# Performance work log

Measured on AMD Instinct MI355X. Metric: run time of the kernel, lower is better.

## Reference

```python
import jax, jax.numpy as jnp
import numpy as np
import math

B, T, M, C = 4, 2048, 16, 256   # batch, seq, m chunks, c_s chunk width
DIM = 1024                       # layer width; k = DIM // C = 4
D = 64                           # conditioning bottleneck
N_ITERS, TAU = 20, 1.0


def _diag_bias(rows, cols):
    b = np.full((rows, cols), -8.0, dtype=np.float32)
    for i in range(min(rows, cols)):
        b[i, i] = 0.0
    return jnp.asarray(b)


def setup_inputs() -> dict:
    key = jax.random.key(0)
    ks = jax.random.split(key, 10)
    state_dim = M * C
    k = DIM // C
    H_post = np.full((M, k), -8.0, dtype=np.float32)
    for i in range(M):
        H_post[i, i % k] = 0.0
    return {
        "s": jax.random.normal(ks[0], (B, T, M, C), jnp.float32),
        "gamma": 0.02 * jax.random.normal(ks[1], (state_dim,), jnp.float32),
        "compress": 0.02 * jax.random.normal(ks[2], (state_dim, D), jnp.float32),
        "alpha_pre": jnp.float32(0.01),
        "to_logits_pre": 0.02 * jax.random.normal(ks[3], (D, k * M), jnp.float32),
        "H_pre": _diag_bias(k, M),
        "alpha_align": jnp.float32(0.01),
        "to_logits_align": 0.02 * jax.random.normal(ks[4], (D, M * M), jnp.float32),
        "H_align": _diag_bias(M, M),
        "alpha_next": jnp.float32(0.01),
        "to_logits_next": 0.02 * jax.random.normal(ks[5], (D, M * M), jnp.float32),
        "H_next": _diag_bias(M, M),
        "alpha_post": jnp.float32(0.01),
        "to_logits_post": 0.02 * jax.random.normal(ks[6], (D, M * k), jnp.float32),
        "H_post": jnp.asarray(H_post),
        "W_layer": jax.random.normal(ks[7], (DIM, DIM), jnp.float32) / math.sqrt(DIM),
    }


def sinkhorn_log(logits, num_iters=N_ITERS, tau=TAU):
    """Log-domain Sinkhorn; output row-scaled so row sums = 1 * rows-normalized."""
    rows, cols = logits.shape[-2], logits.shape[-1]
    Z = logits / tau
    lr = -math.log(rows)
    lc = -math.log(cols)
    u0 = jnp.zeros(Z.shape[:-1], Z.dtype)
    v0 = jnp.zeros(Z.shape[:-2] + (cols,), Z.dtype)

    def body(_, uv):
        u, v = uv
        u = lr - jax.nn.logsumexp(Z + v[..., None, :], axis=-1)
        v = lc - jax.nn.logsumexp(Z + u[..., None], axis=-2)
        return (u, v)

    u, v = jax.lax.fori_loop(0, num_iters, body, (u0, v0))
    return jnp.exp(Z + u[..., None] + v[..., None, :]) * rows


def _route(code, alpha, to_logits, bias, state, rows, cols):
    """Fused: Sinkhorn(alpha*(code@to_logits)+bias) @ state."""
    raw = (code @ to_logits).reshape(code.shape[:-1] + (rows, cols))
    P = sinkhorn_log(alpha * raw + bias)
    return jnp.einsum('...ij,...jc->...ic', P, state)


def reference(s, gamma, compress, alpha_pre, to_logits_pre, H_pre,
              alpha_align, to_logits_align, H_align,
              alpha_next, to_logits_next, H_next,
              alpha_post, to_logits_post, H_post, W_layer):
    b, t, m, c = s.shape
    state_dim = m * c
    k = W_layer.shape[0] // c
    # RMSNorm over flattened state: F.normalize * sqrt(dim) * (gamma + 1)
    s_vec = s.reshape(b, t, state_dim)
    l2 = jnp.sqrt(jnp.sum(s_vec * s_vec, axis=-1, keepdims=True))
    s_norm = s_vec / jnp.maximum(l2, 1e-12) * jnp.sqrt(jnp.float32(state_dim)) * (gamma + 1.0)
    code = s_norm @ compress  # (b, t, d)
    # read: H_pre (k x m) routes state -> layer input
    layer_in = _route(code, alpha_pre, to_logits_pre, H_pre, s, k, m).reshape(b, t, k * c)
    layer_out = layer_in @ W_layer  # the wrapped layer_fn (dense linear)
    # write: align, absorb output via H_post, prepare next via H_next
    s_aligned = _route(code, alpha_align, to_logits_align, H_align, s, m, m)
    out_flat = layer_out.reshape(b, t, k, c)
    s_updated = s_aligned + _route(code, alpha_post, to_logits_post, H_post, out_flat, m, k)
    s_next = _route(code, alpha_next, to_logits_next, H_next, s_updated, m, m)
    return s_next
```

## Files before the change

### kernel.cpp

```cpp
#include <hip/hip_runtime.h>
#include <math.h>

#define NTOK 8192
#define SD   4096
#define ITERS 20

typedef __attribute__((ext_vector_type(8))) short short8;
typedef __attribute__((ext_vector_type(8))) unsigned short ushort8;
typedef __attribute__((ext_vector_type(4))) float f32x4;

__device__ inline unsigned short f2bf(float x) {
    unsigned int u = __float_as_uint(x);
    unsigned int r = (u + 0x7FFFu + ((u >> 16) & 1u)) >> 16;
    return (unsigned short)r;
}

__global__ __launch_bounds__(256) void k_prep(const float* __restrict__ compress,
                                              const float* __restrict__ gamma,
                                              unsigned short* __restrict__ cgT)
{
    __shared__ float tb[64][65];
    __shared__ float gsh[64];
    const int tid = threadIdx.x;
    const int k0 = blockIdx.x * 64;
    #pragma unroll 4
    for (int q = 0; q < 16; ++q) {
        const int idx = q * 256 + tid;
        const int r = idx >> 6, dd = idx & 63;
        tb[r][dd] = compress[(size_t)(k0 + r) * 64 + dd];
    }
    if (tid < 64) gsh[tid] = gamma[k0 + tid] + 1.0f;
    __syncthreads();
    #pragma unroll 4
    for (int q = 0; q < 16; ++q) {
        const int idx = q * 256 + tid;
        const int d = idx >> 6, r = idx & 63;
        cgT[(size_t)d * SD + k0 + r] = f2bf(tb[r][d] * gsh[r]);
    }
}

__global__ __launch_bounds__(256) void k_prept(const float* __restrict__ tl_pre,
                                               const float* __restrict__ tl_al,
                                               const float* __restrict__ tl_nx,
                                               const float* __restrict__ tl_po,
                                               unsigned short* __restrict__ tlT)
{
    const int idx = blockIdx.x * 256 + threadIdx.x;
    if (idx >= 640 * 64) return;
    const int k = idx / 640, n = idx - k * 640;
    float v;
    if (n < 64)       v = tl_pre[k * 64 + n];
    else if (n < 320) v = tl_al[k * 256 + (n - 64)];
    else if (n < 576) v = tl_nx[k * 256 + (n - 320)];
    else              v = tl_po[k * 64 + (n - 576)];
    tlT[(size_t)n * 64 + k] = f2bf(v);
}

__global__ __launch_bounds__(256) void k_code3(const float* __restrict__ s,
                                               const unsigned short* __restrict__ cgT,
                                               unsigned short* __restrict__ codeBF)
{
    __shared__ __align__(16) unsigned short s_sh[32 * 152];
    __shared__ __align__(16) unsigned short cg_sh[64 * 152];
    __shared__ float red[4 * 32 * 68];
    __shared__ float ssq_sh[32];
    const int tid  = threadIdx.x;
    const int lane = tid & 63;
    const int wid  = tid >> 6;
    const int tok0 = blockIdx.x * 32;
    const int st_tok = tid >> 3, st_k = (tid & 7) * 16;
    const int sg_d   = tid >> 2, sg_k = (tid & 3) * 32;
    const int wk = wid * 32;

    float ssq = 0.f;
    f32x4 acc[2][4];
    #pragma unroll
    for (int mi = 0; mi < 2; ++mi)
        #pragma unroll
        for (int ni = 0; ni < 4; ++ni) acc[mi][ni] = (f32x4){0.f, 0.f, 0.f, 0.f};

    for (int ks = 0; ks < 32; ++ks) {
        const int kg = ks * 128;
        __syncthreads();
        {
            const float4* sp = (const float4*)(s + (size_t)(tok0 + st_tok) * SD + kg + st_k);
            float4 v0 = sp[0], v1 = sp[1], v2 = sp[2], v3 = sp[3];
            ssq += v0.x*v0.x + v0.y*v0.y + v0.z*v0.z + v0.w*v0.w
                 + v1.x*v1.x + v1.y*v1.y + v1.z*v1.z + v1.w*v1.w
                 + v2.x*v2.x + v2.y*v2.y + v2.z*v2.z + v2.w*v2.w
                 + v3.x*v3.x + v3.y*v3.y + v3.z*v3.z + v3.w*v3.w;
            ushort8 lo, hi;
            lo[0]=f2bf(v0.x); lo[1]=f2bf(v0.y); lo[2]=f2bf(v0.z); lo[3]=f2bf(v0.w);
            lo[4]=f2bf(v1.x); lo[5]=f2bf(v1.y); lo[6]=f2bf(v1.z); lo[7]=f2bf(v1.w);
            hi[0]=f2bf(v2.x); hi[1]=f2bf(v2.y); hi[2]=f2bf(v2.z); hi[3]=f2bf(v2.w);
            hi[4]=f2bf(v3.x); hi[5]=f2bf(v3.y); hi[6]=f2bf(v3.z); hi[7]=f2bf(v3.w);
            ushort8* sw = (ushort8*)(s_sh + st_tok * 152 + st_k);
            sw[0] = lo; sw[1] = hi;
        }
        {
            const ushort8* gp = (const ushort8*)(cgT + (size_t)sg_d * SD + kg + sg_k);
            ushort8 c0 = gp[0], c1 = gp[1], c2 = gp[2], c3 = gp[3];
            ushort8* cw = (ushort8*)(cg_sh + sg_d * 152 + sg_k);
            cw[0] = c0; cw[1] = c1; cw[2] = c2; cw[3] = c3;
        }
        __syncthreads();

        short8 a[2], b[4];
        #pragma unroll
        for (int mi = 0; mi < 2; ++mi)
            a[mi] = *(const short8*)(s_sh + (mi * 16 + (lane & 15)) * 152 + wk + (lane >> 4) * 8);
        #pragma unroll
        for (int ni = 0; ni < 4; ++ni)
            b[ni] = *(const short8*)(cg_sh + (ni * 16 + (lane & 15)) * 152 + wk + (lane >> 4) * 8);
        #pragma unroll
        for (int mi = 0; mi < 2; ++mi)
            #pragma unroll
            for (int ni = 0; ni < 4; ++ni)
                acc[mi][ni] = __builtin_amdgcn_mfma_f32_16x16x32_bf16(a[mi], b[ni], acc[mi][ni], 0, 0, 0);
    }

    ssq += __shfl_xor(ssq, 1);
    ssq += __shfl_xor(ssq, 2);
    ssq += __shfl_xor(ssq, 4);
    if ((tid & 7) == 0) ssq_sh[st_tok] = ssq;

    #pragma unroll
    for (int mi = 0; mi < 2; ++mi)
        #pragma unroll
        for (int ni = 0; ni < 4; ++ni)
            #pragma unroll
            for (int r = 0; r < 4; ++r)
                red[wid * 2176 + (mi * 16 + (lane >> 4) * 4 + r) * 68 + ni * 16 + (lane & 15)] = acc[mi][ni][r];
    __syncthreads();
    if (tid < 32) ssq_sh[tid] = 64.0f / fmaxf(sqrtf(ssq_sh[tid]), 1e-12f);
    __syncthreads();

    #pragma unroll
    for (int q = 0; q < 8; ++q) {
        const int idx = q * 256 + tid;
        const int tok = idx >> 6, d = idx & 63;
        float v = red[0 * 2176 + tok * 68 + d] + red[1 * 2176 + tok * 68 + d]
                + red[2 * 2176 + tok * 68 + d] + red[3 * 2176 + tok * 68 + d];
        codeBF[(size_t)(tok0 + tok) * 64 + d] = f2bf(v * ssq_sh[tok]);
    }
}

__global__ __launch_bounds__(256) void k_logits(const unsigned short* __restrict__ codeBF,
                                                const unsigned short* __restrict__ tlT,
                                                float* __restrict__ logits)
{
    const int tid  = threadIdx.x;
    const int lane = tid & 63;
    const int wid  = tid >> 6;
    const int m0 = blockIdx.y * 64 + wid * 16;
    const int n0 = blockIdx.x * 128;

    f32x4 acc[8];
    #pragma unroll
    for (int ni = 0; ni < 8; ++ni) acc[ni] = (f32x4){0.f, 0.f, 0.f, 0.f};

    #pragma unroll
    for (int ks = 0; ks < 2; ++ks) {
        const int ko = ks * 32 + (lane >> 4) * 8;
        short8 a = *(const short8*)(codeBF + (size_t)(m0 + (lane & 15)) * 64 + ko);
        short8 b[8];
        #pragma unroll
        for (int ni = 0; ni < 8; ++ni)
            b[ni] = *(const short8*)(tlT + (size_t)(n0 + ni * 16 + (lane & 15)) * 64 + ko);
        #pragma unroll
        for (int ni = 0; ni < 8; ++ni)
            acc[ni] = __builtin_amdgcn_mfma_f32_16x16x32_bf16(a, b[ni], acc[ni], 0, 0, 0);
    }
    #pragma unroll
    for (int ni = 0; ni < 8; ++ni)
        #pragma unroll
        for (int r = 0; r < 4; ++r)
            logits[(size_t)(m0 + (lane >> 4) * 4 + r) * 640 + n0 + ni * 16 + (lane & 15)] = acc[ni][r];
}

__global__ __launch_bounds__(256) void k_sink(const float* __restrict__ logits,
                                              const float* __restrict__ a_pre_p, const float* __restrict__ H_pre,
                                              const float* __restrict__ a_al_p,  const float* __restrict__ H_al,
                                              const float* __restrict__ a_nx_p,  const float* __restrict__ H_nx,
                                              const float* __restrict__ a_po_p,  const float* __restrict__ H_po,
                                              float* __restrict__ Ppre,
                                              float* __restrict__ Pna, float* __restrict__ Pnp)
{
    __shared__ float Pal_sh[16 * 260];
    __shared__ float Pnx_sh[16 * 260];
    __shared__ float Ppo_sh[16 * 68];
    const int tid  = threadIdx.x;
    const int lane = tid & 63;
    const int wid  = tid >> 6;
    const int tok0 = blockIdx.x * 16;
    const int t_in = lane >> 2;
    const int sub  = lane & 3;
    const int tok  = tok0 + t_in;

    if (wid < 2) {
        const float alpha = (wid == 0) ? (*a_al_p) : (*a_nx_p);
        const float* Hp   = ((wid == 0) ? H_al : H_nx) + sub * 64;
        const float* lgp  = logits + (size_t)tok * 640 + (wid == 0 ? 64 : 320) + sub * 64;
        float Km[4][16];
        #pragma unroll
        for (int rr = 0; rr < 4; ++rr)
            #pragma unroll
            for (int c4 = 0; c4 < 4; ++c4) {
                float4 rv = *(const float4*)(lgp + rr * 16 + c4 * 4);
                float4 hv = *(const float4*)(Hp  + rr * 16 + c4 * 4);
                Km[rr][c4*4+0] = expf(alpha * rv.x + hv.x);
                Km[rr][c4*4+1] = expf(alpha * rv.y + hv.y);
                Km[rr][c4*4+2] = expf(alpha * rv.z + hv.z);
                Km[rr][c4*4+3] = expf(alpha * rv.w + hv.w);
            }
        float v[16], u[4];
        #pragma unroll
        for (int c = 0; c < 16; ++c) v[c] = 1.0f;
        for (int it = 0; it < ITERS; ++it) {
            #pragma unroll
            for (int rr = 0; rr < 4; ++rr) {
                float su = 0.f;
                #pragma unroll
                for (int c = 0; c < 16; ++c) su += Km[rr][c] * v[c];
                u[rr] = 0.0625f * __builtin_amdgcn_rcpf(su);
            }
            float pv[16];
            #pragma unroll
            for (int c = 0; c < 16; ++c)
                pv[c] = Km[0][c]*u[0] + Km[1][c]*u[1] + Km[2][c]*u[2] + Km[3][c]*u[3];
            #pragma unroll
            for (int c = 0; c < 16; ++c) pv[c] += __shfl_xor(pv[c], 1);
            #pragma unroll
            for (int c = 0; c < 16; ++c) pv[c] += __shfl_xor(pv[c], 2);
            #pragma unroll
            for (int c = 0; c < 16; ++c) v[c] = 0.0625f * __builtin_amdgcn_rcpf(pv[c]);
        }
        float* dst = ((wid == 0) ? Pal_sh : Pnx_sh) + t_in * 260;
        #pragma unroll
        for (int rr = 0; rr < 4; ++rr) {
            const float su16 = 16.0f * u[rr];
            #pragma unroll
            for (int c = 0; c < 16; ++c)
                dst[(sub * 4 + rr) * 16 + c] = Km[rr][c] * su16 * v[c];
        }
    } else if (wid == 2) {
        const float alpha = *a_pre_p;
        const float* lgp = logits + (size_t)tok * 640 + sub * 16;
        const float* Hp  = H_pre + sub * 16;
        float Km[16];
        #pragma unroll
        for (int c4 = 0; c4 < 4; ++c4) {
            float4 rv = *(const float4*)(lgp + c4 * 4);
            float4 hv = *(const float4*)(Hp  + c4 * 4);
            Km[c4*4+0] = expf(alpha * rv.x + hv.x);
            Km[c4*4+1] = expf(alpha * rv.y + hv.y);
            Km[c4*4+2] = expf(alpha * rv.z + hv.z);
            Km[c4*4+3] = expf(alpha * rv.w + hv.w);
        }
        float v[16], u;
        #pragma unroll
        for (int c = 0; c < 16; ++c) v[c] = 1.0f;
        for (int it = 0; it < ITERS; ++it) {
            float su = 0.f;
            #pragma unroll
            for (int c = 0; c < 16; ++c) su += Km[c] * v[c];
            u = 0.25f * __builtin_amdgcn_rcpf(su);
            float pv[16];
            #pragma unroll
            for (int c = 0; c < 16; ++c) pv[c] = Km[c] * u;
            #pragma unroll
            for (int c = 0; c < 16; ++c) pv[c] += __shfl_xor(pv[c], 1);
            #pragma unroll
            for (int c = 0; c < 16; ++c) pv[c] += __shfl_xor(pv[c], 2);
            #pragma unroll
            for (int c = 0; c < 16; ++c) v[c] = 0.0625f * __builtin_amdgcn_rcpf(pv[c]);
        }
        const float su4 = 4.0f * u;
        #pragma unroll
        for (int c = 0; c < 16; ++c)
            Ppre[(size_t)tok * 64 + sub * 16 + c] = Km[c] * su4 * v[c];
    } else {
        const float alpha = *a_po_p;
        const float* lgp = logits + (size_t)tok * 640 + 576 + sub * 16;
        const float* Hp  = H_po + sub * 16;
        float Km[4][4];
        #pragma unroll
        for (int rr = 0; rr < 4; ++rr) {
            float4 rv = *(const float4*)(lgp + rr * 4);
            float4 hv = *(const float4*)(Hp  + rr * 4);
            Km[rr][0] = expf(alpha * rv.x + hv.x);
            Km[rr][1] = expf(alpha * rv.y + hv.y);
            Km[rr][2] = expf(alpha * rv.z + hv.z);
            Km[rr][3] = expf(alpha * rv.w + hv.w);
        }
        float v[4], u[4];
        #pragma unroll
        for (int c = 0; c < 4; ++c) v[c] = 1.0f;
        for (int it = 0; it < ITERS; ++it) {
            #pragma unroll
            for (int rr = 0; rr < 4; ++rr) {
                float su = 0.f;
                #pragma unroll
                for (int c = 0; c < 4; ++c) su += Km[rr][c] * v[c];
                u[rr] = 0.0625f * __builtin_amdgcn_rcpf(su);
            }
            float pv[4];
            #pragma unroll
            for (int c = 0; c < 4; ++c)
                pv[c] = Km[0][c]*u[0] + Km[1][c]*u[1] + Km[2][c]*u[2] + Km[3][c]*u[3];
            #pragma unroll
            for (int c = 0; c < 4; ++c) pv[c] += __shfl_xor(pv[c], 1);
            #pragma unroll
            for (int c = 0; c < 4; ++c) pv[c] += __shfl_xor(pv[c], 2);
            #pragma unroll
            for (int c = 0; c < 4; ++c) v[c] = 0.25f * __builtin_amdgcn_rcpf(pv[c]);
        }
        #pragma unroll
        for (int rr = 0; rr < 4; ++rr) {
            const float su16 = 16.0f * u[rr];
            #pragma unroll
            for (int c = 0; c < 4; ++c)
                Ppo_sh[t_in * 68 + (sub * 4 + rr) * 4 + c] = Km[rr][c] * su16 * v[c];
        }
    }
    __syncthreads();

    const int ct = tid >> 4;
    const int cj = tid & 15;
    const float* pnx = Pnx_sh + ct * 260;
    const float* pal = Pal_sh + ct * 260;
    const float* ppo = Ppo_sh + ct * 68;
    #pragma unroll
    for (int m = 0; m < 16; ++m) {
        float acc = 0.f;
        #pragma unroll
        for (int t2 = 0; t2 < 16; ++t2) acc += pnx[m * 16 + t2] * pal[t2 * 16 + cj];
        Pna[(size_t)(tok0 + ct) * 256 + m * 16 + cj] = acc;
    }
    #pragma unroll
    for (int e = 0; e < 4; ++e) {
        const int idx = cj * 4 + e;
        const int m = idx >> 2, q = idx & 3;
        float acc = 0.f;
        #pragma unroll
        for (int t2 = 0; t2 < 16; ++t2) acc += pnx[m * 16 + t2] * ppo[t2 * 4 + q];
        Pnp[(size_t)(tok0 + ct) * 64 + idx] = acc;
    }
}

__global__ __launch_bounds__(256) void k_apply(const float* __restrict__ s,
                                               const float* __restrict__ Ppre,
                                               unsigned short* __restrict__ layer_in)
{
    __shared__ float Ppre_sh[64];
    const int tid = threadIdx.x;
    const int tok = blockIdx.x;
    float sreg[16];
    #pragma unroll
    for (int j = 0; j < 16; ++j) sreg[j] = s[(size_t)tok * SD + j * 256 + tid];
    if (tid < 64) Ppre_sh[tid] = Ppre[(size_t)tok * 64 + tid];
    __syncthreads();
    #pragma unroll
    for (int i = 0; i < 4; ++i) {
        float acc = 0.f;
        #pragma unroll
        for (int j = 0; j < 16; ++j) acc += Ppre_sh[i * 16 + j] * sreg[j];
        layer_in[(size_t)tok * 1024 + i * 256 + tid] = f2bf(acc);
    }
}

__global__ __launch_bounds__(256) void k_wt(const float* __restrict__ W,
                                            unsigned short* __restrict__ WT)
{
    __shared__ float tb[64][65];
    const int k0 = blockIdx.y * 64, n0 = blockIdx.x * 64;
    #pragma unroll 4
    for (int q = 0; q < 16; ++q) {
        const int idx = q * 256 + threadIdx.x;
        const int r = idx >> 6, c = idx & 63;
        tb[r][c] = W[(size_t)(k0 + r) * 1024 + n0 + c];
    }
    __syncthreads();
    #pragma unroll 4
    for (int q = 0; q < 16; ++q) {
        const int idx = q * 256 + threadIdx.x;
        const int n = idx >> 6, k = idx & 63;
        WT[(size_t)(n0 + n) * 1024 + k0 + k] = f2bf(tb[k][n]);
    }
}

__global__ __launch_bounds__(256) void k_gemm_bf16(const unsigned short* __restrict__ A,
                                                   const unsigned short* __restrict__ BT,
                                                   float* __restrict__ C)
{
    __shared__ unsigned short Abuf[128 * 48];
    __shared__ unsigned short Bbuf[128 * 48];
    const int tid  = threadIdx.x;
    const int lane = tid & 63;
    const int wid  = tid >> 6;
    const int wr   = wid >> 1, wc = wid & 1;
    const int m0 = blockIdx.y * 128, n0 = blockIdx.x * 128;

    f32x4 acc[4][4];
    #pragma unroll
    for (int mi = 0; mi < 4; ++mi)
        #pragma unroll
        for (int ni = 0; ni < 4; ++ni) acc[mi][ni] = (f32x4){0.f, 0.f, 0.f, 0.f};

    for (int k0 = 0; k0 < 1024; k0 += 32) {
        __syncthreads();
        #pragma unroll
        for (int h = 0; h < 2; ++h) {
            const int idx = h * 256 + tid;
            const int row = idx >> 2, kq = idx & 3;
            float4 av = *(const float4*)(A + (size_t)(m0 + row) * 1024 + k0 + kq * 8);
            *(float4*)(Abuf + row * 48 + kq * 8) = av;
            float4 bv = *(const float4*)(BT + (size_t)(n0 + row) * 1024 + k0 + kq * 8);
            *(float4*)(Bbuf + row * 48 + kq * 8) = bv;
        }
        __syncthreads();

        short8 a[4], b[4];
        #pragma unroll
        for (int mi = 0; mi < 4; ++mi)
            a[mi] = *(const short8*)(Abuf + (wr * 64 + mi * 16 + (lane & 15)) * 48 + (lane >> 4) * 8);
        #pragma unroll
        for (int ni = 0; ni < 4; ++ni)
            b[ni] = *(const short8*)(Bbuf + (wc * 64 + ni * 16 + (lane & 15)) * 48 + (lane >> 4) * 8);
        #pragma unroll
        for (int mi = 0; mi < 4; ++mi)
            #pragma unroll
            for (int ni = 0; ni < 4; ++ni)
                acc[mi][ni] = __builtin_amdgcn_mfma_f32_16x16x32_bf16(a[mi], b[ni], acc[mi][ni], 0, 0, 0);
    }

    #pragma unroll
    for (int mi = 0; mi < 4; ++mi)
        #pragma unroll
        for (int ni = 0; ni < 4; ++ni)
            #pragma unroll
            for (int r = 0; r < 4; ++r)
                C[(size_t)(m0 + wr * 64 + mi * 16 + (lane >> 4) * 4 + r) * 1024 +
                  n0 + wc * 64 + ni * 16 + (lane & 15)] = acc[mi][ni][r];
}

__global__ __launch_bounds__(256) void k_final(const float* __restrict__ s,
                                               const float* __restrict__ lo,
                                               const float* __restrict__ Pna,
                                               const float* __restrict__ Pnp,
                                               float* __restrict__ out)
{
    __shared__ float s_sh[SD];
    __shared__ float lo_sh[1024];
    __shared__ float Pna_sh[256];
    __shared__ float Pnp_sh[64];
    const int tid = threadIdx.x;
    const int tok = blockIdx.x;

    {
        const float4* sp4 = (const float4*)(s + (size_t)tok * SD);
        float4* d4 = (float4*)s_sh;
        #pragma unroll
        for (int j = 0; j < 4; ++j) d4[j * 256 + tid] = sp4[j * 256 + tid];
        ((float4*)lo_sh)[tid] = ((const float4*)(lo + (size_t)tok * 1024))[tid];
        Pna_sh[tid] = Pna[(size_t)tok * 256 + tid];
        if (tid < 64) Pnp_sh[tid] = Pnp[(size_t)tok * 64 + tid];
    }
    __syncthreads();

    const int c = tid;
    #pragma unroll
    for (int m = 0; m < 16; ++m) {
        float acc = 0.f;
        #pragma unroll
        for (int j = 0; j < 16; ++j) acc += Pna_sh[m * 16 + j] * s_sh[j * 256 + c];
        #pragma unroll
        for (int q = 0; q < 4; ++q) acc += Pnp_sh[m * 4 + q] * lo_sh[q * 256 + c];
        out[(size_t)tok * SD + m * 256 + c] = acc;
    }
}

extern "C" void kernel_launch(void* const* d_in, const int* in_sizes, int n_in,
                              void* d_out, int out_size, void* d_ws, size_t ws_size,
                              hipStream_t stream)
{
    const float* s        = (const float*)d_in[0];
    const float* gamma    = (const float*)d_in[1];
    const float* compress = (const float*)d_in[2];
    const float* a_pre    = (const float*)d_in[3];
    const float* tl_pre   = (const float*)d_in[4];
    const float* H_pre    = (const float*)d_in[5];
    const float* a_al     = (const float*)d_in[6];
    const float* tl_al    = (const float*)d_in[7];
    const float* H_al     = (const float*)d_in[8];
    const float* a_nx     = (const float*)d_in[9];
    const float* tl_nx    = (const float*)d_in[10];
    const float* H_nx     = (const float*)d_in[11];
    const float* a_po     = (const float*)d_in[12];
    const float* tl_po    = (const float*)d_in[13];
    const float* H_po     = (const float*)d_in[14];
    const float* W        = (const float*)d_in[15];
    float* out = (float*)d_out;

    float* layer_out         = (float*)d_ws;
    float* logits            = layer_out;
    float* Pna               = layer_out + (size_t)8192 * 1024;
    float* Pnp               = Pna + (size_t)8192 * 256;
    unsigned short* layer_in = (unsigned short*)(Pnp + (size_t)8192 * 64);
    unsigned short* WT       = layer_in + (size_t)8192 * 1024;
    unsigned short* cgT      = WT + (size_t)1024 * 1024;
    unsigned short* codeBF   = cgT + (size_t)64 * SD;
    unsigned short* tlT      = codeBF + (size_t)8192 * 64;
    float* Ppre              = (float*)(tlT + (size_t)640 * 64 + 64);

    k_wt<<<dim3(16, 16), 256, 0, stream>>>(W, WT);
    k_prep<<<64, 256, 0, stream>>>(compress, gamma, cgT);
    k_prept<<<160, 256, 0, stream>>>(tl_pre, tl_al, tl_nx, tl_po, tlT);
    k_code3<<<256, 256, 0, stream>>>(s, cgT, codeBF);
    k_logits<<<dim3(5, 128), 256, 0, stream>>>(codeBF, tlT, logits);
    k_sink<<<512, 256, 0, stream>>>(logits,
                                    a_pre, H_pre, a_al, H_al,
                                    a_nx, H_nx, a_po, H_po,
                                    Ppre, Pna, Pnp);
    k_apply<<<NTOK, 256, 0, stream>>>(s, Ppre, layer_in);
    k_gemm_bf16<<<dim3(8, 64), 256, 0, stream>>>(layer_in, WT, layer_out);
    k_final<<<NTOK, 256, 0, stream>>>(s, layer_out, Pna, Pnp, out);
}
```

Baseline: 213.7 us.

## Cache bf16 copy of state for later passes and emit bf16 layer output

The code-projection kernel now also writes a bf16 copy of the state tensor, when the workspace is large enough. The apply and final kernels then read that half-size copy instead of the fp32 state, and the GEMM writes its output in bf16 rather than fp32. This cuts global memory traffic in the bandwidth-bound per-token kernels. The final output is now built from bf16-rounded state and layer output, which adds error. The code kernel also moves to 16-token tiles with twice as many blocks, and k_apply stages the state through shared memory.

```diff
diff --git a/kernel.cpp b/kernel.cpp
--- a/kernel.cpp
+++ b/kernel.cpp
@@ -7,12 +7,16 @@
 
 typedef __attribute__((ext_vector_type(8))) short short8;
 typedef __attribute__((ext_vector_type(8))) unsigned short ushort8;
+typedef __attribute__((ext_vector_type(4))) unsigned short us4;
 typedef __attribute__((ext_vector_type(4))) float f32x4;
 
 __device__ inline unsigned short f2bf(float x) {
     unsigned int u = __float_as_uint(x);
     unsigned int r = (u + 0x7FFFu + ((u >> 16) & 1u)) >> 16;
     return (unsigned short)r;
+}
+__device__ inline float bf2f(unsigned short u) {
+    return __uint_as_float((unsigned int)u << 16);
 }
 
 __global__ __launch_bounds__(256) void k_prep(const float* __restrict__ compress,
@@ -56,46 +60,64 @@
     tlT[(size_t)n * 64 + k] = f2bf(v);
 }
 
-__global__ __launch_bounds__(256) void k_code3(const float* __restrict__ s,
+__global__ __launch_bounds__(256) void k_wt(const float* __restrict__ W,
+                                            unsigned short* __restrict__ WT)
+{
+    __shared__ float tb[64][65];
+    const int k0 = blockIdx.y * 64, n0 = blockIdx.x * 64;
+    #pragma unroll 4
+    for (int q = 0; q < 16; ++q) {
+        const int idx = q * 256 + threadIdx.x;
+        const int r = idx >> 6, c = idx & 63;
+        tb[r][c] = W[(size_t)(k0 + r) * 1024 + n0 + c];
+    }
+    __syncthreads();
+    #pragma unroll 4
+    for (int q = 0; q < 16; ++q) {
+        const int idx = q * 256 + threadIdx.x;
+        const int n = idx >> 6, k = idx & 63;
+        WT[(size_t)(n0 + n) * 1024 + k0 + k] = f2bf(tb[k][n]);
+    }
+}
+
+__global__ __launch_bounds__(256) void k_code4(const float* __restrict__ s,
                                                const unsigned short* __restrict__ cgT,
-                                               unsigned short* __restrict__ codeBF)
-{
-    __shared__ __align__(16) unsigned short s_sh[32 * 152];
+                                               unsigned short* __restrict__ codeBF,
+                                               unsigned short* __restrict__ s_bf)
+{
+    __shared__ __align__(16) unsigned short s_sh[16 * 152];
     __shared__ __align__(16) unsigned short cg_sh[64 * 152];
-    __shared__ float red[4 * 32 * 68];
-    __shared__ float ssq_sh[32];
+    __shared__ float red[4 * 16 * 68];
+    __shared__ float ssq_sh[16];
     const int tid  = threadIdx.x;
     const int lane = tid & 63;
     const int wid  = tid >> 6;
-    const int tok0 = blockIdx.x * 32;
-    const int st_tok = tid >> 3, st_k = (tid & 7) * 16;
-    const int sg_d   = tid >> 2, sg_k = (tid & 3) * 32;
+    const int tok0 = blockIdx.x * 16;
+    const int st_tok = tid >> 4;
+    const int st_k   = (tid & 15) * 8;
+    const int sg_d   = tid >> 2;
+    const int sg_k   = (tid & 3) * 32;
     const int wk = wid * 32;
 
     float ssq = 0.f;
-    f32x4 acc[2][4];
-    #pragma unroll
-    for (int mi = 0; mi < 2; ++mi)
-        #pragma unroll
-        for (int ni = 0; ni < 4; ++ni) acc[mi][ni] = (f32x4){0.f, 0.f, 0.f, 0.f};
+    f32x4 acc[4];
+    #pragma unroll
+    for (int ni = 0; ni < 4; ++ni) acc[ni] = (f32x4){0.f, 0.f, 0.f, 0.f};
 
     for (int ks = 0; ks < 32; ++ks) {
         const int kg = ks * 128;
         __syncthreads();
         {
             const float4* sp = (const float4*)(s + (size_t)(tok0 + st_tok) * SD + kg + st_k);
-            float4 v0 = sp[0], v1 = sp[1], v2 = sp[2], v3 = sp[3];
+            float4 v0 = sp[0], v1 = sp[1];
             ssq += v0.x*v0.x + v0.y*v0.y + v0.z*v0.z + v0.w*v0.w
-                 + v1.x*v1.x + v1.y*v1.y + v1.z*v1.z + v1.w*v1.w
-                 + v2.x*v2.x + v2.y*v2.y + v2.z*v2.z + v2.w*v2.w
-                 + v3.x*v3.x + v3.y*v3.y + v3.z*v3.z + v3.w*v3.w;
-            ushort8 lo, hi;
-            lo[0]=f2bf(v0.x); lo[1]=f2bf(v0.y); lo[2]=f2bf(v0.z); lo[3]=f2bf(v0.w);
-            lo[4]=f2bf(v1.x); lo[5]=f2bf(v1.y); lo[6]=f2bf(v1.z); lo[7]=f2bf(v1.w);
-            hi[0]=f2bf(v2.x); hi[1]=f2bf(v2.y); hi[2]=f2bf(v2.z); hi[3]=f2bf(v2.w);
-            hi[4]=f2bf(v3.x); hi[5]=f2bf(v3.y); hi[6]=f2bf(v3.z); hi[7]=f2bf(v3.w);
-            ushort8* sw = (ushort8*)(s_sh + st_tok * 152 + st_k);
-            sw[0] = lo; sw[1] = hi;
+                 + v1.x*v1.x + v1.y*v1.y + v1.z*v1.z + v1.w*v1.w;
+            ushort8 pk;
+            pk[0]=f2bf(v0.x); pk[1]=f2bf(v0.y); pk[2]=f2bf(v0.z); pk[3]=f2bf(v0.w);
+            pk[4]=f2bf(v1.x); pk[5]=f2bf(v1.y); pk[6]=f2bf(v1.z); pk[7]=f2bf(v1.w);
+            *(ushort8*)(s_sh + st_tok * 152 + st_k) = pk;
+            if (s_bf)
+                *(ushort8*)(s_bf + (size_t)(tok0 + st_tok) * SD + kg + st_k) = pk;
         }
         {
             const ushort8* gp = (const ushort8*)(cgT + (size_t)sg_d * SD + kg + sg_k);
@@ -105,42 +127,37 @@
         }
         __syncthreads();
 
-        short8 a[2], b[4];
-        #pragma unroll
-        for (int mi = 0; mi < 2; ++mi)
-            a[mi] = *(const short8*)(s_sh + (mi * 16 + (lane & 15)) * 152 + wk + (lane >> 4) * 8);
+        short8 a = *(const short8*)(s_sh + (lane & 15) * 152 + wk + (lane >> 4) * 8);
+        short8 b[4];
         #pragma unroll
         for (int ni = 0; ni < 4; ++ni)
             b[ni] = *(const short8*)(cg_sh + (ni * 16 + (lane & 15)) * 152 + wk + (lane >> 4) * 8);
         #pragma unroll
-        for (int mi = 0; mi < 2; ++mi)
-            #pragma unroll
-            for (int ni = 0; ni < 4; ++ni)
-                acc[mi][ni] = __builtin_amdgcn_mfma_f32_16x16x32_bf16(a[mi], b[ni], acc[mi][ni], 0, 0, 0);
+        for (int ni = 0; ni < 4; ++ni)
+            acc[ni] = __builtin_amdgcn_mfma_f32_16x16x32_bf16(a, b[ni], acc[ni], 0, 0, 0);
     }
 
     ssq += __shfl_xor(ssq, 1);
     ssq += __shfl_xor(ssq, 2);
     ssq += __shfl_xor(ssq, 4);
-    if ((tid & 7) == 0) ssq_sh[st_tok] = ssq;
-
-    #pragma unroll
-    for (int mi = 0; mi < 2; ++mi)
-        #pragma unroll
-        for (int ni = 0; ni < 4; ++ni)
-            #pragma unroll
-            for (int r = 0; r < 4; ++r)
-                red[wid * 2176 + (mi * 16 + (lane >> 4) * 4 + r) * 68 + ni * 16 + (lane & 15)] = acc[mi][ni][r];
-    __syncthreads();
-    if (tid < 32) ssq_sh[tid] = 64.0f / fmaxf(sqrtf(ssq_sh[tid]), 1e-12f);
-    __syncthreads();
-
-    #pragma unroll
-    for (int q = 0; q < 8; ++q) {
+    ssq += __shfl_xor(ssq, 8);
+    if ((tid & 15) == 0) ssq_sh[st_tok] = ssq;
+
+    #pragma unroll
+    for (int ni = 0; ni < 4; ++ni)
+        #pragma unroll
+        for (int r = 0; r < 4; ++r)
+            red[wid * 1088 + ((lane >> 4) * 4 + r) * 68 + ni * 16 + (lane & 15)] = acc[ni][r];
+    __syncthreads();
+    if (tid < 16) ssq_sh[tid] = 64.0f / fmaxf(sqrtf(ssq_sh[tid]), 1e-12f);
+    __syncthreads();
+
+    #pragma unroll
+    for (int q = 0; q < 4; ++q) {
         const int idx = q * 256 + tid;
         const int tok = idx >> 6, d = idx & 63;
-        float v = red[0 * 2176 + tok * 68 + d] + red[1 * 2176 + tok * 68 + d]
-                + red[2 * 2176 + tok * 68 + d] + red[3 * 2176 + tok * 68 + d];
+        float v = red[0 * 1088 + tok * 68 + d] + red[1 * 1088 + tok * 68 + d]
+                + red[2 * 1088 + tok * 68 + d] + red[3 * 1088 + tok * 68 + d];
         codeBF[(size_t)(tok0 + tok) * 64 + d] = f2bf(v * ssq_sh[tok]);
     }
 }
@@ -348,50 +365,48 @@
     }
 }
 
-__global__ __launch_bounds__(256) void k_apply(const float* __restrict__ s,
-                                               const float* __restrict__ Ppre,
-                                               unsigned short* __restrict__ layer_in)
-{
-    __shared__ float Ppre_sh[64];
+template<bool SBF>
+__global__ __launch_bounds__(256) void k_apply2(const float* __restrict__ s,
+                                                const unsigned short* __restrict__ s_bf,
+                                                const float* __restrict__ Ppre,
+                                                unsigned short* __restrict__ layer_in)
+{
+    __shared__ float s_sh[SD];
+    __shared__ float P_sh[64];
     const int tid = threadIdx.x;
     const int tok = blockIdx.x;
-    float sreg[16];
-    #pragma unroll
-    for (int j = 0; j < 16; ++j) sreg[j] = s[(size_t)tok * SD + j * 256 + tid];
-    if (tid < 64) Ppre_sh[tid] = Ppre[(size_t)tok * 64 + tid];
-    __syncthreads();
+
+    if (SBF) {
+        #pragma unroll
+        for (int c2 = 0; c2 < 2; ++c2) {
+            ushort8 v = *(const ushort8*)(s_bf + (size_t)tok * SD + c2 * 2048 + tid * 8);
+            float4 f0, f1;
+            f0.x = bf2f(v[0]); f0.y = bf2f(v[1]); f0.z = bf2f(v[2]); f0.w = bf2f(v[3]);
+            f1.x = bf2f(v[4]); f1.y = bf2f(v[5]); f1.z = bf2f(v[6]); f1.w = bf2f(v[7]);
+            *(float4*)(s_sh + c2 * 2048 + tid * 8)     = f0;
+            *(float4*)(s_sh + c2 * 2048 + tid * 8 + 4) = f1;
+        }
+    } else {
+        const float4* sp4 = (const float4*)(s + (size_t)tok * SD);
+        #pragma unroll
+        for (int j = 0; j < 4; ++j)
+            *(float4*)(s_sh + j * 1024 + tid * 4) = sp4[j * 256 + tid];
+    }
+    if (tid < 64) P_sh[tid] = Ppre[(size_t)tok * 64 + tid];
+    __syncthreads();
+
     #pragma unroll
     for (int i = 0; i < 4; ++i) {
         float acc = 0.f;
         #pragma unroll
-        for (int j = 0; j < 16; ++j) acc += Ppre_sh[i * 16 + j] * sreg[j];
+        for (int j = 0; j < 16; ++j) acc += P_sh[i * 16 + j] * s_sh[j * 256 + tid];
         layer_in[(size_t)tok * 1024 + i * 256 + tid] = f2bf(acc);
-    }
-}
-
-__global__ __launch_bounds__(256) void k_wt(const float* __restrict__ W,
-                                            unsigned short* __restrict__ WT)
-{
-    __shared__ float tb[64][65];
-    const int k0 = blockIdx.y * 64, n0 = blockIdx.x * 64;
-    #pragma unroll 4
-    for (int q = 0; q < 16; ++q) {
-        const int idx = q * 256 + threadIdx.x;
-        const int r = idx >> 6, c = idx & 63;
-        tb[r][c] = W[(size_t)(k0 + r) * 1024 + n0 + c];
-    }
-    __syncthreads();
-    #pragma unroll 4
-    for (int q = 0; q < 16; ++q) {
-        const int idx = q * 256 + threadIdx.x;
-        const int n = idx >> 6, k = idx & 63;
-        WT[(size_t)(n0 + n) * 1024 + k0 + k] = f2bf(tb[k][n]);
     }
 }
 
 __global__ __launch_bounds__(256) void k_gemm_bf16(const unsigned short* __restrict__ A,
                                                    const unsigned short* __restrict__ BT,
-                                                   float* __restrict__ C)
+                                                   unsigned short* __restrict__ Cb)
 {
     __shared__ unsigned short Abuf[128 * 48];
     __shared__ unsigned short Bbuf[128 * 48];
@@ -440,15 +455,17 @@
         for (int ni = 0; ni < 4; ++ni)
             #pragma unroll
             for (int r = 0; r < 4; ++r)
-                C[(size_t)(m0 + wr * 64 + mi * 16 + (lane >> 4) * 4 + r) * 1024 +
-                  n0 + wc * 64 + ni * 16 + (lane & 15)] = acc[mi][ni][r];
-}
-
-__global__ __launch_bounds__(256) void k_final(const float* __restrict__ s,
-                                               const float* __restrict__ lo,
-                                               const float* __restrict__ Pna,
-                                               const float* __restrict__ Pnp,
-                                               float* __restrict__ out)
+                Cb[(size_t)(m0 + wr * 64 + mi * 16 + (lane >> 4) * 4 + r) * 1024 +
+                   n0 + wc * 64 + ni * 16 + (lane & 15)] = f2bf(acc[mi][ni][r]);
+}
+
+template<bool SBF>
+__global__ __launch_bounds__(256) void k_final2(const float* __restrict__ s,
+                                                const unsigned short* __restrict__ s_bf,
+                                                const unsigned short* __restrict__ lo_bf,
+                                                const float* __restrict__ Pna,
+                                                const float* __restrict__ Pnp,
+                                                float* __restrict__ out)
 {
     __shared__ float s_sh[SD];
     __shared__ float lo_sh[1024];
@@ -457,15 +474,30 @@
     const int tid = threadIdx.x;
     const int tok = blockIdx.x;
 
+    if (SBF) {
+        #pragma unroll
+        for (int c2 = 0; c2 < 2; ++c2) {
+            ushort8 v = *(const ushort8*)(s_bf + (size_t)tok * SD + c2 * 2048 + tid * 8);
+            float4 f0, f1;
+            f0.x = bf2f(v[0]); f0.y = bf2f(v[1]); f0.z = bf2f(v[2]); f0.w = bf2f(v[3]);
+            f1.x = bf2f(v[4]); f1.y = bf2f(v[5]); f1.z = bf2f(v[6]); f1.w = bf2f(v[7]);
+            *(float4*)(s_sh + c2 * 2048 + tid * 8)     = f0;
+            *(float4*)(s_sh + c2 * 2048 + tid * 8 + 4) = f1;
+        }
+    } else {
+        const float4* sp4 = (const float4*)(s + (size_t)tok * SD);
+        #pragma unroll
+        for (int j = 0; j < 4; ++j)
+            *(float4*)(s_sh + j * 1024 + tid * 4) = sp4[j * 256 + tid];
+    }
     {
-        const float4* sp4 = (const float4*)(s + (size_t)tok * SD);
-        float4* d4 = (float4*)s_sh;
-        #pragma unroll
-        for (int j = 0; j < 4; ++j) d4[j * 256 + tid] = sp4[j * 256 + tid];
-        ((float4*)lo_sh)[tid] = ((const float4*)(lo + (size_t)tok * 1024))[tid];
-        Pna_sh[tid] = Pna[(size_t)tok * 256 + tid];
-        if (tid < 64) Pnp_sh[tid] = Pnp[(size_t)tok * 64 + tid];
-    }
+        us4 lv = *(const us4*)(lo_bf + (size_t)tok * 1024 + tid * 4);
+        float4 f;
+        f.x = bf2f(lv[0]); f.y = bf2f(lv[1]); f.z = bf2f(lv[2]); f.w = bf2f(lv[3]);
+        *(float4*)(lo_sh + tid * 4) = f;
+    }
+    Pna_sh[tid] = Pna[(size_t)tok * 256 + tid];
+    if (tid < 64) Pnp_sh[tid] = Pnp[(size_t)tok * 64 + tid];
     __syncthreads();
 
     const int c = tid;
@@ -502,27 +534,39 @@
     const float* W        = (const float*)d_in[15];
     float* out = (float*)d_out;
 
-    float* layer_out         = (float*)d_ws;
+    char* p = (char*)d_ws;
+    float* layer_out         = (float*)p;          p += (size_t)8192 * 1024 * 4;
     float* logits            = layer_out;
-    float* Pna               = layer_out + (size_t)8192 * 1024;
-    float* Pnp               = Pna + (size_t)8192 * 256;
-    unsigned short* layer_in = (unsigned short*)(Pnp + (size_t)8192 * 64);
-    unsigned short* WT       = layer_in + (size_t)8192 * 1024;
-    unsigned short* cgT      = WT + (size_t)1024 * 1024;
-    unsigned short* codeBF   = cgT + (size_t)64 * SD;
-    unsigned short* tlT      = codeBF + (size_t)8192 * 64;
-    float* Ppre              = (float*)(tlT + (size_t)640 * 64 + 64);
+    unsigned short* lo_bf    = (unsigned short*)layer_out;
+    float* Pna               = (float*)p;          p += (size_t)8192 * 256 * 4;
+    float* Pnp               = (float*)p;          p += (size_t)8192 * 64 * 4;
+    unsigned short* layer_in = (unsigned short*)p; p += (size_t)8192 * 1024 * 2;
+    unsigned short* WT       = (unsigned short*)p; p += (size_t)1024 * 1024 * 2;
+    unsigned short* cgT      = (unsigned short*)p; p += (size_t)64 * SD * 2;
+    unsigned short* codeBF   = (unsigned short*)p; p += (size_t)8192 * 64 * 2;
+    unsigned short* tlT      = (unsigned short*)p; p += (size_t)640 * 64 * 2 + 128;
+    float* Ppre              = (float*)p;          p += (size_t)8192 * 64 * 4;
+    unsigned short* s_bf     = (unsigned short*)p; p += (size_t)NTOK * SD * 2;
+    const bool use_sbf = ((size_t)(p - (char*)d_ws) <= ws_size);
 
     k_wt<<<dim3(16, 16), 256, 0, stream>>>(W, WT);
     k_prep<<<64, 256, 0, stream>>>(compress, gamma, cgT);
     k_prept<<<160, 256, 0, stream>>>(tl_pre, tl_al, tl_nx, tl_po, tlT);
-    k_code3<<<256, 256, 0, stream>>>(s, cgT, codeBF);
+    k_code4<<<512, 256, 0, stream>>>(s, cgT, codeBF, use_sbf ? s_bf : (unsigned short*)nullptr);
     k_logits<<<dim3(5, 128), 256, 0, stream>>>(codeBF, tlT, logits);
     k_sink<<<512, 256, 0, stream>>>(logits,
                                     a_pre, H_pre, a_al, H_al,
                                     a_nx, H_nx, a_po, H_po,
                                     Ppre, Pna, Pnp);
-    k_apply<<<NTOK, 256, 0, stream>>>(s, Ppre, layer_in);
-    k_gemm_bf16<<<dim3(8, 64), 256, 0, stream>>>(layer_in, WT, layer_out);
-    k_final<<<NTOK, 256, 0, stream>>>(s, layer_out, Pna, Pnp, out);
-}
+    if (use_sbf) {
+        k_apply2<true><<<NTOK, 256, 0, stream>>>(s, s_bf, Ppre, layer_in);
+    } else {
+        k_apply2<false><<<NTOK, 256, 0, stream>>>(s, s_bf, Ppre, layer_in);
+    }
+    k_gemm_bf16<<<dim3(8, 64), 256, 0, stream>>>(layer_in, WT, lo_bf);
+    if (use_sbf) {
+        k_final2<true><<<NTOK, 256, 0, stream>>>(s, s_bf, lo_bf, Pna, Pnp, out);
+    } else {
+        k_final2<false><<<NTOK, 256, 0, stream>>>(s, s_bf, lo_bf, Pna, Pnp, out);
+    }
+}
```

Measured after the change: 214.5 us. No clear change (+0.4%).
